# Optimization experiments

Measured on AMD Instinct MI355X. Metric: run time of the kernel, lower is better.

Reference implementation:

```python
import jax, jax.numpy as jnp
import numpy as np

B = 2048
IN_DIM = 8192
OUT_DIM = 16384
N_GATES = 16


def setup_inputs() -> dict:
    key = jax.random.key(0)
    k1, k2, k3, k4 = jax.random.split(key, 4)
    x = jax.random.uniform(k1, (B, IN_DIM), dtype=jnp.float32)  # values in [0,1]
    logits = jax.random.normal(k2, (OUT_DIM, N_GATES), dtype=jnp.float32)  # init_std=1.0
    # fixed random connectivity: permutation trick from _pairwise_random_connections
    perm = jax.random.permutation(k3, 2 * OUT_DIM) % IN_DIM
    perm = jax.random.permutation(k4, IN_DIM)[perm]
    c = perm.reshape(2, OUT_DIM)
    return {
        "x": x,
        "logits": logits,
        "a_idx": c[0].astype(jnp.int32),
        "b_idx": c[1].astype(jnp.int32),
    }


def _bin_op_s(a, b, p):
    # a, b: (B, out_dim); p: (out_dim, 16) gate probabilities, broadcast over batch.
    # Weighted sum of the 16 real-valued relaxations of 2-input Boolean gates
    # (standard DiffLogic gate ordering; gate 0 is constant 0, gate 15 constant 1).
    ab = a * b
    return (
        p[:, 1] * ab                          # AND
        + p[:, 2] * (a - ab)                  # a AND NOT b
        + p[:, 3] * a                         # a
        + p[:, 4] * (b - ab)                  # NOT a AND b
        + p[:, 5] * b                         # b
        + p[:, 6] * (a + b - 2.0 * ab)        # XOR
        + p[:, 7] * (a + b - ab)              # OR
        + p[:, 8] * (1.0 - (a + b - ab))      # NOR
        + p[:, 9] * (1.0 - (a + b - 2.0 * ab))  # XNOR
        + p[:, 10] * (1.0 - b)                # NOT b
        + p[:, 11] * (1.0 - b + ab)           # a OR NOT b
        + p[:, 12] * (1.0 - a)                # NOT a
        + p[:, 13] * (1.0 - a + ab)           # NOT a OR b
        + p[:, 14] * (1.0 - ab)               # NAND
        + p[:, 15]                            # constant 1
    )


def reference(x, logits, a_idx, b_idx):
    # Gather the two inputs of each output gate: (B, out_dim)
    a = x[:, a_idx]
    b = x[:, b_idx]
    # Training mode: softmax relaxation over the 16 gates per node.
    p = jax.nn.softmax(logits, axis=-1)
    return _bin_op_s(a, b, p)
```

## Files before the change

kernel.cpp:

```cpp
#include <hip/hip_runtime.h>
#include <hip/hip_bf16.h>

#define IN_DIM  8192
#define OUT_DIM 16384
#define BATCH   2048
#define NG      16
#define CHUNKS  2
#define RROWS   2
#define TPB     512
#define NITER   (OUT_DIM / CHUNKS / 4 / TPB)

typedef float        f32x4 __attribute__((ext_vector_type(4)));
typedef unsigned int u32x4 __attribute__((ext_vector_type(4)));


__device__ __forceinline__ void collapse_weights(const float* __restrict__ l,
                                                 float& w_ab, float& w_a,
                                                 float& w_b, float& w_c) {
    float v[NG];
    float m = -1e30f;
#pragma unroll
    for (int k = 0; k < NG; ++k) { v[k] = l[k]; m = fmaxf(m, v[k]); }
    float s = 0.f;
#pragma unroll
    for (int k = 0; k < NG; ++k) { v[k] = __expf(v[k] - m); s += v[k]; }
    float inv = 1.0f / s;
#pragma unroll
    for (int k = 0; k < NG; ++k) v[k] *= inv;
    w_ab = v[1] - v[2] - v[4] - 2.f * v[6] - v[7] + v[8] + 2.f * v[9]
         + v[11] + v[13] - v[14];
    w_a  = v[2] + v[3] + v[6] + v[7] - v[8] - v[9] - v[12] - v[13];
    w_b  = v[4] + v[5] + v[6] + v[7] - v[8] - v[9] - v[10] - v[11];
    w_c  = v[8] + v[9] + v[10] + v[11] + v[12] + v[13] + v[14] + v[15];
}

__global__ __launch_bounds__(256) void gate_weights_kernel(
    const float* __restrict__ logits,
    const int* __restrict__ a_idx, const int* __restrict__ b_idx,
    float* __restrict__ ws) {
    int j = blockIdx.x * blockDim.x + threadIdx.x;
    if (j >= OUT_DIM) return;
    float w_ab, w_a, w_b, w_c;
    collapse_weights(logits + (size_t)j * NG, w_ab, w_a, w_b, w_c);
    ws[j]               = w_ab;
    ws[j +     OUT_DIM] = w_a;
    ws[j + 2 * OUT_DIM] = w_b;
    ws[j + 3 * OUT_DIM] = w_c;
    unsigned int* pk = (unsigned int*)(ws + 4 * OUT_DIM);
    pk[j] = (unsigned int)a_idx[j] | ((unsigned int)b_idx[j] << 16);
}

__global__ __launch_bounds__(TPB, 4) void gate_eval_kernel(
    const float* __restrict__ x,
    const float* __restrict__ ws,
    f32x4* __restrict__ out4) {
    __shared__ float rows[RROWS * IN_DIM];
    const int bid   = blockIdx.x;
    const int ipair = bid >> 1;
    const int chunk = bid & 1;
    const int i0    = ipair * RROWS;

    const f32x4* wab4 = (const f32x4*)(ws);
    const f32x4* wa4  = (const f32x4*)(ws + OUT_DIM);
    const f32x4* wb4  = (const f32x4*)(ws + 2 * OUT_DIM);
    const f32x4* wc4  = (const f32x4*)(ws + 3 * OUT_DIM);
    const u32x4* pk4  = (const u32x4*)(ws + 4 * OUT_DIM);
    const int base4 = chunk * (OUT_DIM / CHUNKS / 4);

    u32x4 pkb[2];
    f32x4 wabb[2], wab_[2], wbb[2], wcb[2];
    {
        int j4 = base4 + threadIdx.x;
        pkb[0]  = pk4[j4];
        wabb[0] = wab4[j4];
        wab_[0] = wa4[j4];
        wbb[0]  = wb4[j4];
        wcb[0]  = wc4[j4];
    }

    const f32x4* xr = (const f32x4*)(x + (size_t)i0 * IN_DIM);
    f32x4* rv = (f32x4*)rows;
#pragma unroll
    for (int t = 0; t < RROWS * IN_DIM / 4 / TPB; ++t)
        rv[threadIdx.x + t * TPB] = xr[threadIdx.x + t * TPB];
    __syncthreads();

    f32x4* o0 = out4 + (size_t)i0 * (OUT_DIM / 4);
    f32x4* o1 = o0 + (OUT_DIM / 4);

#pragma unroll
    for (int k = 0; k < NITER; ++k) {
        const int cur = k & 1, nxt = cur ^ 1;
        if (k + 1 < NITER) {
            int j4n = base4 + threadIdx.x + (k + 1) * TPB;
            pkb[nxt]  = pk4[j4n];
            wabb[nxt] = wab4[j4n];
            wab_[nxt] = wa4[j4n];
            wbb[nxt]  = wb4[j4n];
            wcb[nxt]  = wc4[j4n];
        }
        int j4 = base4 + threadIdx.x + k * TPB;
        u32x4 pk = pkb[cur];
        f32x4 wab = wabb[cur], wa = wab_[cur], wb = wbb[cur], wc = wcb[cur];
        f32x4 r0, r1;
#pragma unroll
        for (int c = 0; c < 4; ++c) {
            int ia = (int)(pk[c] & 0xFFFFu);
            int ib = (int)(pk[c] >> 16);
            float a0 = rows[ia],          b0 = rows[ib];
            float a1 = rows[ia + IN_DIM], b1 = rows[ib + IN_DIM];
            r0[c] = fmaf(wab[c], a0 * b0, fmaf(wa[c], a0, fmaf(wb[c], b0, wc[c])));
            r1[c] = fmaf(wab[c], a1 * b1, fmaf(wa[c], a1, fmaf(wb[c], b1, wc[c])));
        }
        __builtin_nontemporal_store(r0, &o0[j4]);
        __builtin_nontemporal_store(r1, &o1[j4]);
    }
}

__global__ __launch_bounds__(256) void gate_eval_fused_kernel(
    const float* __restrict__ x,
    const float* __restrict__ logits,
    const int* __restrict__ a_idx,
    const int* __restrict__ b_idx,
    float* __restrict__ out) {
    __shared__ float row[IN_DIM];
    const int i = blockIdx.x;
    const f32x4* xr = (const f32x4*)(x + (size_t)i * IN_DIM);
    f32x4* rv = (f32x4*)row;
#pragma unroll
    for (int t = 0; t < IN_DIM / 4 / 256; ++t)
        rv[threadIdx.x + t * 256] = xr[threadIdx.x + t * 256];
    __syncthreads();
    float* o = out + (size_t)i * OUT_DIM;
    for (int k = 0; k < OUT_DIM / 256; ++k) {
        int j = threadIdx.x + k * 256;
        float w_ab, w_a, w_b, w_c;
        collapse_weights(logits + (size_t)j * NG, w_ab, w_a, w_b, w_c);
        float a = row[a_idx[j]], b = row[b_idx[j]];
        o[j] = fmaf(w_ab, a * b, fmaf(w_a, a, fmaf(w_b, b, w_c)));
    }
}

extern "C" void kernel_launch(void* const* d_in, const int* in_sizes, int n_in,
                              void* d_out, int out_size, void* d_ws, size_t ws_size,
                              hipStream_t stream) {
    const float* x      = (const float*)d_in[0];
    const float* logits = (const float*)d_in[1];
    const int*   a_idx  = (const int*)d_in[2];
    const int*   b_idx  = (const int*)d_in[3];
    float* out = (float*)d_out;

    const size_t ws_need = (size_t)(4 * OUT_DIM) * sizeof(float)
                         + (size_t)OUT_DIM * sizeof(unsigned int);
    if (ws_size >= ws_need && d_ws != nullptr) {
        float* ws = (float*)d_ws;
        gate_weights_kernel<<<OUT_DIM / 256, 256, 0, stream>>>(
            logits, a_idx, b_idx, ws);
        gate_eval_kernel<<<(BATCH / RROWS) * CHUNKS, TPB, 0, stream>>>(
            x, ws, (f32x4*)out);
    } else {
        gate_eval_fused_kernel<<<BATCH, 256, 0, stream>>>(
            x, logits, a_idx, b_idx, out);
    }
}
```

Baseline: 49.35 us.

## Interleave two batch rows in LDS as float2 and drop output chunking

```diff
diff --git a/kernel.cpp b/kernel.cpp
--- a/kernel.cpp
+++ b/kernel.cpp
@@ -5,11 +5,11 @@
 #define OUT_DIM 16384
 #define BATCH   2048
 #define NG      16
-#define CHUNKS  2
 #define RROWS   2
 #define TPB     512
-#define NITER   (OUT_DIM / CHUNKS / 4 / TPB)
+#define NITER   (OUT_DIM / 4 / TPB)
 
+typedef float        f32x2 __attribute__((ext_vector_type(2)));
 typedef float        f32x4 __attribute__((ext_vector_type(4)));
 typedef unsigned int u32x4 __attribute__((ext_vector_type(4)));
 
@@ -54,23 +54,19 @@
     const float* __restrict__ x,
     const float* __restrict__ ws,
     f32x4* __restrict__ out4) {
-    __shared__ float rows[RROWS * IN_DIM];
-    const int bid   = blockIdx.x;
-    const int ipair = bid >> 1;
-    const int chunk = bid & 1;
-    const int i0    = ipair * RROWS;
+    __shared__ f32x2 rows2[IN_DIM];
+    const int i0 = blockIdx.x * RROWS;
 
     const f32x4* wab4 = (const f32x4*)(ws);
     const f32x4* wa4  = (const f32x4*)(ws + OUT_DIM);
     const f32x4* wb4  = (const f32x4*)(ws + 2 * OUT_DIM);
     const f32x4* wc4  = (const f32x4*)(ws + 3 * OUT_DIM);
     const u32x4* pk4  = (const u32x4*)(ws + 4 * OUT_DIM);
-    const int base4 = chunk * (OUT_DIM / CHUNKS / 4);
 
     u32x4 pkb[2];
     f32x4 wabb[2], wab_[2], wbb[2], wcb[2];
     {
-        int j4 = base4 + threadIdx.x;
+        int j4 = threadIdx.x;
         pkb[0]  = pk4[j4];
         wabb[0] = wab4[j4];
         wab_[0] = wa4[j4];
@@ -78,11 +74,19 @@
         wcb[0]  = wc4[j4];
     }
 
-    const f32x4* xr = (const f32x4*)(x + (size_t)i0 * IN_DIM);
-    f32x4* rv = (f32x4*)rows;
+    const f32x4* xr0 = (const f32x4*)(x + (size_t)i0 * IN_DIM);
+    const f32x4* xr1 = (const f32x4*)(x + (size_t)(i0 + 1) * IN_DIM);
 #pragma unroll
-    for (int t = 0; t < RROWS * IN_DIM / 4 / TPB; ++t)
-        rv[threadIdx.x + t * TPB] = xr[threadIdx.x + t * TPB];
+    for (int t = 0; t < IN_DIM / 4 / TPB; ++t) {
+        int m = threadIdx.x + t * TPB;
+        f32x4 r0 = xr0[m];
+        f32x4 r1 = xr1[m];
+#pragma unroll
+        for (int c = 0; c < 4; ++c) {
+            f32x2 p; p.x = r0[c]; p.y = r1[c];
+            rows2[m * 4 + c] = p;
+        }
+    }
     __syncthreads();
 
     f32x4* o0 = out4 + (size_t)i0 * (OUT_DIM / 4);
@@ -92,25 +96,25 @@
     for (int k = 0; k < NITER; ++k) {
         const int cur = k & 1, nxt = cur ^ 1;
         if (k + 1 < NITER) {
-            int j4n = base4 + threadIdx.x + (k + 1) * TPB;
+            int j4n = threadIdx.x + (k + 1) * TPB;
             pkb[nxt]  = pk4[j4n];
             wabb[nxt] = wab4[j4n];
             wab_[nxt] = wa4[j4n];
             wbb[nxt]  = wb4[j4n];
             wcb[nxt]  = wc4[j4n];
         }
-        int j4 = base4 + threadIdx.x + k * TPB;
+        int j4 = threadIdx.x + k * TPB;
         u32x4 pk = pkb[cur];
         f32x4 wab = wabb[cur], wa = wab_[cur], wb = wbb[cur], wc = wcb[cur];
         f32x4 r0, r1;
 #pragma unroll
         for (int c = 0; c < 4; ++c) {
-            int ia = (int)(pk[c] & 0xFFFFu);
-            int ib = (int)(pk[c] >> 16);
-            float a0 = rows[ia],          b0 = rows[ib];
-            float a1 = rows[ia + IN_DIM], b1 = rows[ib + IN_DIM];
-            r0[c] = fmaf(wab[c], a0 * b0, fmaf(wa[c], a0, fmaf(wb[c], b0, wc[c])));
-            r1[c] = fmaf(wab[c], a1 * b1, fmaf(wa[c], a1, fmaf(wb[c], b1, wc[c])));
+            f32x2 va = rows2[pk[c] & 0xFFFFu];
+            f32x2 vb = rows2[pk[c] >> 16];
+            r0[c] = fmaf(wab[c], va.x * vb.x,
+                         fmaf(wa[c], va.x, fmaf(wb[c], vb.x, wc[c])));
+            r1[c] = fmaf(wab[c], va.y * vb.y,
+                         fmaf(wa[c], va.y, fmaf(wb[c], vb.y, wc[c])));
         }
         __builtin_nontemporal_store(r0, &o0[j4]);
         __builtin_nontemporal_store(r1, &o1[j4]);
@@ -156,7 +160,7 @@
         float* ws = (float*)d_ws;
         gate_weights_kernel<<<OUT_DIM / 256, 256, 0, stream>>>(
             logits, a_idx, b_idx, ws);
-        gate_eval_kernel<<<(BATCH / RROWS) * CHUNKS, TPB, 0, stream>>>(
+        gate_eval_kernel<<<BATCH / RROWS, TPB, 0, stream>>>(
             x, ws, (f32x4*)out);
     } else {
         gate_eval_fused_kernel<<<BATCH, 256, 0, stream>>>(
```

Measured after the change: 40.03 us. 18.9% less time.
